# Kernel optimization log

Hardware: AMD Instinct MI355X
Metric: run time of the kernel (lower is better)

## Reference

```python
import jax, jax.numpy as jnp
import numpy as np

B, C, H, W = 2, 512, 64, 64


def conv1x1(x, w, b):
    # x: [B,C,H,W], w: [O,C], b: [O]
    return jnp.einsum('bchw,oc->bohw', x, w) + b[None, :, None, None]


def setup_inputs() -> dict:
    key = jax.random.key(0)
    ks = jax.random.split(key, 20)
    d = {
        'visSegF': jax.random.normal(ks[0], (B, C, H, W), jnp.float32),
        'irSegF': jax.random.normal(ks[1], (B, C, H, W), jnp.float32),
        'x_vis_p': jax.random.normal(ks[2], (B, C, H, W), jnp.float32),
        'x_ir_p': jax.random.normal(ks[3], (B, C, H, W), jnp.float32),
    }
    names = ['q_rd', 'k_rd', 'v_rd', 'q_dr', 'k_dr', 'v_dr']
    for i, n in enumerate(names):
        d['W' + n] = jax.random.normal(ks[4 + 2 * i], (C, C), jnp.float32) * 0.02
        d['b' + n] = jax.random.normal(ks[5 + 2 * i], (C,), jnp.float32) * 0.01
    # gamma params are init-zero in torch; use small nonzero values so both paths contribute
    d['gamma_rd'] = jax.random.normal(ks[16], (1,), jnp.float32) * 0.1
    d['gamma_dr'] = jax.random.normal(ks[17], (1,), jnp.float32) * 0.1
    return d


def reference(visSegF, irSegF, x_vis_p, x_ir_p,
              Wq_rd, bq_rd, Wk_rd, bk_rd, Wv_rd, bv_rd,
              Wq_dr, bq_dr, Wk_dr, bk_dr, Wv_dr, bv_dr,
              gamma_rd, gamma_dr):
    b, c, h, w = x_vis_p.shape
    n = h * w

    # rd path: query from x_vis_p, key from visSegF, value from x_ir_p (sr_ratio == 1 branch)
    q_vis = conv1x1(x_vis_p, Wq_rd, bq_rd).reshape(b, c, n)      # [B,C,N]
    key_d = conv1x1(visSegF, Wk_rd, bk_rd).reshape(b, c, -1)     # [B,C,M]
    val_d = conv1x1(x_ir_p, Wv_rd, bv_rd).reshape(b, c, -1)      # [B,C,M]
    # torch: softmax(bmm(q^T, k), dim=1) -> softmax over query positions (axis=1)
    attn_rd = jax.nn.softmax(jnp.einsum('bcn,bcm->bnm', q_vis, key_d), axis=1)
    out_rd = jnp.einsum('bcm,bnm->bcn', val_d, attn_rd).reshape(b, c, h, w)

    # dr path: query from x_ir_p, key/value from irSegF
    q_ir = conv1x1(x_ir_p, Wq_dr, bq_dr).reshape(b, c, n)
    key_r = conv1x1(irSegF, Wk_dr, bk_dr).reshape(b, c, -1)
    val_r = conv1x1(irSegF, Wv_dr, bv_dr).reshape(b, c, -1)
    attn_dr = jax.nn.softmax(jnp.einsum('bcn,bcm->bnm', q_ir, key_r), axis=1)
    out_dr = jnp.einsum('bcm,bnm->bcn', val_r, attn_dr).reshape(b, c, h, w)

    out_rd = jax.nn.relu(gamma_rd[0] * out_rd + x_vis_p)
    out_dr = jax.nn.relu(gamma_dr[0] * out_dr + x_ir_p)
    return (out_rd, out_dr)
```

## Files before the change

### kernel.cpp

```cpp
#include <hip/hip_runtime.h>
#include <stdint.h>


typedef __attribute__((ext_vector_type(8))) __bf16 bf16x8;
typedef __attribute__((ext_vector_type(4))) float f32x4;

__device__ __forceinline__ unsigned short f2bf(float f) {
  union { float f; unsigned u; } v; v.f = f;
  unsigned r = v.u + 0x7FFFu + ((v.u >> 16) & 1u);
  return (unsigned short)(r >> 16);
}
__device__ __forceinline__ float bf2f(unsigned short b) {
  union { unsigned u; float f; } v; v.u = ((unsigned)b) << 16;
  return v.f;
}

__device__ __forceinline__ void async_copy16(const unsigned short* g,
                                             unsigned short* l) {
  __builtin_amdgcn_global_load_lds(
      (const __attribute__((address_space(1))) unsigned int*)g,
      (__attribute__((address_space(3))) unsigned int*)l, 16, 0, 0);
}

template <int NSUB>
__device__ __forceinline__ void gemm_core(
    const unsigned short* __restrict__ Ag, const unsigned short* __restrict__ Bg,
    int K, int lda, int ldb, int rowbase, int colbase,
    f32x4 (&acc)[4][4], unsigned short* Al, unsigned short* Bl) {
  const int tid = threadIdx.x;
  const int w = tid >> 6, lane = tid & 63;
  const int quad = lane >> 4, l16 = lane & 15;
  const int wm = (w >> 1) << 6, wn = (w & 1) << 6;
  const int rbase = (w << 5) + (lane >> 2);

  for (int k0 = 0; k0 < K; k0 += 32 * NSUB) {
#pragma unroll
    for (int half = 0; half < NSUB; ++half) {
      int kh = k0 + (half << 5);
      unsigned short* Ah = Al + (half << 12);
      unsigned short* Bh = Bl + (half << 12);
#pragma unroll
      for (int i = 0; i < 2; ++i) {
        int rloc = rbase + (i << 4);
        int cg = (lane & 3) ^ ((rloc >> 1) & 3);
        int koff = kh + (cg << 3);
        int ldsoff = ((w << 5) + (i << 4)) << 5;
        async_copy16(Ag + (size_t)(rowbase + rloc) * lda + koff, Ah + ldsoff);
        async_copy16(Bg + (size_t)(colbase + rloc) * ldb + koff, Bh + ldsoff);
      }
    }
    __syncthreads();
#pragma unroll
    for (int half = 0; half < NSUB; ++half) {
      unsigned short* Ah = Al + (half << 12);
      unsigned short* Bh = Bl + (half << 12);
      bf16x8 af[4], bfr[4];
#pragma unroll
      for (int i = 0; i < 4; ++i) {
        int r = wm + (i << 4) + l16;
        af[i] = *(const bf16x8*)(Ah + (r << 5) + ((quad ^ ((r >> 1) & 3)) << 3));
      }
#pragma unroll
      for (int j = 0; j < 4; ++j) {
        int r = wn + (j << 4) + l16;
        bfr[j] = *(const bf16x8*)(Bh + (r << 5) + ((quad ^ ((r >> 1) & 3)) << 3));
      }
#pragma unroll
      for (int i = 0; i < 4; ++i)
#pragma unroll
        for (int j = 0; j < 4; ++j)
          acc[i][j] = __builtin_amdgcn_mfma_f32_16x16x32_bf16(af[i], bfr[j], acc[i][j], 0, 0, 0);
    }
    __syncthreads();
  }
}

struct WArgs { const float* src[6]; unsigned short* dst[6]; };
__global__ __launch_bounds__(256) void k_cvtw(WArgs a) {
  int z = blockIdx.y;
  int i = (blockIdx.x * 256 + threadIdx.x) << 3;
  const float* s = a.src[z] + i;
  float4 v0 = *(const float4*)s;
  float4 v1 = *(const float4*)(s + 4);
  unsigned short pk[8] = {f2bf(v0.x), f2bf(v0.y), f2bf(v0.z), f2bf(v0.w),
                          f2bf(v1.x), f2bf(v1.y), f2bf(v1.z), f2bf(v1.w)};
  *(int4*)(a.dst[z] + i) = *(int4*)pk;
}

struct TArgs { const float* src[4]; unsigned short* dst[4]; };
__global__ __launch_bounds__(256) void k_tcvt(TArgs a) {
  __shared__ float tile[32][68];
  int z = blockIdx.z;
  const float* src = a.src[z >> 1] + (size_t)(z & 1) * (512 * 4096);
  unsigned short* dst = a.dst[z >> 1] + (size_t)(z & 1) * (4096 * 512);
  int n0 = blockIdx.x << 6;
  int c0 = blockIdx.y << 5;
  int tid = threadIdx.x;
  int q = tid & 15, r0 = tid >> 4;
#pragma unroll
  for (int pass = 0; pass < 2; ++pass) {
    int r = r0 + (pass << 4);
    *(float4*)&tile[r][q << 2] =
        *(const float4*)(src + (size_t)(c0 + r) * 4096 + n0 + (q << 2));
  }
  __syncthreads();
  int j = tid >> 2, c8 = (tid & 3) << 3;
  unsigned short pk[8];
#pragma unroll
  for (int k = 0; k < 8; ++k) pk[k] = f2bf(tile[c8 + k][j]);
  *(int4*)(dst + (size_t)(n0 + j) * 512 + c0 + c8) = *(int4*)pk;
}

struct ConvArgs {
  const unsigned short* W[12];
  const unsigned short* X[12];
  const float* bias[12];
  unsigned short* out[12];
  int trans[12];
};
__global__ __launch_bounds__(256) void k_conv(ConvArgs a) {
  __shared__ unsigned short sh[16384];
  int z = blockIdx.z;
  int trans = a.trans[z];
  int rowbase = (trans ? blockIdx.x : blockIdx.y) << 7;
  int colbase = (trans ? blockIdx.y : blockIdx.x) << 7;
  const unsigned short* Ag = trans ? a.X[z] : a.W[z];
  const unsigned short* Bg = trans ? a.W[z] : a.X[z];
  f32x4 acc[4][4];
#pragma unroll
  for (int i = 0; i < 4; ++i)
#pragma unroll
    for (int j = 0; j < 4; ++j) acc[i][j] = (f32x4){0.f, 0.f, 0.f, 0.f};
  gemm_core<2>(Ag, Bg, 512, 512, 512, rowbase, colbase, acc, sh, sh + 8192);

  const int tid = threadIdx.x, w = tid >> 6, lane = tid & 63;
  const int quad = lane >> 4, l16 = lane & 15;
  const int wm = (w >> 1) << 6, wn = (w & 1) << 6;
  const float* bias = a.bias[z];
  unsigned short* out = a.out[z];
  if (trans) {
    float bo[4];
#pragma unroll
    for (int j = 0; j < 4; ++j) bo[j] = bias[colbase + wn + (j << 4) + l16];
#pragma unroll
    for (int i = 0; i < 4; ++i) {
      int n0 = rowbase + wm + (i << 4) + (quad << 2);
#pragma unroll
      for (int j = 0; j < 4; ++j) {
        int o = colbase + wn + (j << 4) + l16;
        out[(size_t)(n0 + 0) * 512 + o] = f2bf(acc[i][j].x + bo[j]);
        out[(size_t)(n0 + 1) * 512 + o] = f2bf(acc[i][j].y + bo[j]);
        out[(size_t)(n0 + 2) * 512 + o] = f2bf(acc[i][j].z + bo[j]);
        out[(size_t)(n0 + 3) * 512 + o] = f2bf(acc[i][j].w + bo[j]);
      }
    }
  } else {
#pragma unroll
    for (int i = 0; i < 4; ++i) {
      int o0 = rowbase + wm + (i << 4) + (quad << 2);
      float b0 = bias[o0], b1 = bias[o0 + 1], b2 = bias[o0 + 2], b3 = bias[o0 + 3];
#pragma unroll
      for (int j = 0; j < 4; ++j) {
        int n = colbase + wn + (j << 4) + l16;
        out[(size_t)(o0 + 0) * 4096 + n] = f2bf(acc[i][j].x + b0);
        out[(size_t)(o0 + 1) * 4096 + n] = f2bf(acc[i][j].y + b1);
        out[(size_t)(o0 + 2) * 4096 + n] = f2bf(acc[i][j].z + b2);
        out[(size_t)(o0 + 3) * 4096 + n] = f2bf(acc[i][j].w + b3);
      }
    }
  }
}

struct QKArgs {
  const unsigned short* Q[4]; const unsigned short* K[4]; unsigned short* T[4];
  float* pz;
};
__global__ __launch_bounds__(256) void k_qk(QKArgs a) {
  __shared__ unsigned short sh[16384];
  int z = blockIdx.z;
  int nbase = blockIdx.y << 7;
  int mbase = blockIdx.x << 7;
  f32x4 acc[4][4];
#pragma unroll
  for (int i = 0; i < 4; ++i)
#pragma unroll
    for (int j = 0; j < 4; ++j) acc[i][j] = (f32x4){0.f, 0.f, 0.f, 0.f};
  gemm_core<2>(a.Q[z], a.K[z], 512, 512, 512, nbase, mbase, acc, sh, sh + 8192);

  const int tid = threadIdx.x, w = tid >> 6, lane = tid & 63;
  const int quad = lane >> 4, l16 = lane & 15;
  const int wm = (w >> 1) << 6, wn = (w & 1) << 6;
  unsigned short* T = a.T[z];
  float sjv[4] = {0.f, 0.f, 0.f, 0.f};
#pragma unroll
  for (int i = 0; i < 4; ++i) {
    int n0 = nbase + wm + (i << 4) + (quad << 2);
#pragma unroll
    for (int j = 0; j < 4; ++j) {
      int m = mbase + wn + (j << 4) + l16;
      float e0 = __expf(acc[i][j].x);
      float e1 = __expf(acc[i][j].y);
      float e2 = __expf(acc[i][j].z);
      float e3 = __expf(acc[i][j].w);
      T[(size_t)(n0 + 0) * 4096 + m] = f2bf(e0);
      T[(size_t)(n0 + 1) * 4096 + m] = f2bf(e1);
      T[(size_t)(n0 + 2) * 4096 + m] = f2bf(e2);
      T[(size_t)(n0 + 3) * 4096 + m] = f2bf(e3);
      sjv[j] += e0 + e1 + e2 + e3;
    }
  }
  float* red = (float*)sh;
#pragma unroll
  for (int j = 0; j < 4; ++j) {
    float s = sjv[j];
    s += __shfl_xor(s, 16, 64);
    s += __shfl_xor(s, 32, 64);
    if (quad == 0) red[(w << 6) + (j << 4) + l16] = s;
  }
  __syncthreads();
  if (tid < 128) {
    int h = tid >> 6, t = tid & 63;
    float S = red[(h << 6) + t] + red[((h + 2) << 6) + t];
    int m = mbase + (h << 6) + t;
    a.pz[((z << 5) + blockIdx.y) * 4096 + m] = S;
  }
}

__global__ __launch_bounds__(256) void k_stats2(const float* __restrict__ pz,
                                                float* __restrict__ c) {
  int m = (blockIdx.x << 8) + threadIdx.x;
  int z = blockIdx.y;
  float S = 0.f;
#pragma unroll
  for (int k = 0; k < 32; ++k) S += pz[((z << 5) + k) * 4096 + m];
  c[z * 4096 + m] = 1.f / S;
}

struct VSArgs { unsigned short* V[4]; const float* c; };
__global__ __launch_bounds__(256) void k_vscale(VSArgs a) {
  int z = blockIdx.y;
  int t = blockIdx.x * 256 + threadIdx.x;
  int m0 = (t & 511) << 3;
  int row = t >> 9;
  unsigned short* p = a.V[z] + (size_t)row * 4096 + m0;
  const float* cz = a.c + z * 4096 + m0;
  int4 raw = *(const int4*)p;
  unsigned short* u = (unsigned short*)&raw;
#pragma unroll
  for (int j = 0; j < 8; ++j) u[j] = f2bf(bf2f(u[j]) * cz[j]);
  *(int4*)p = raw;
}

struct PVArgs {
  const unsigned short* V[4];
  const unsigned short* P[4];
  const float* resid[4];
  const float* gamma[4];
  float* out[4];
};
__global__ __launch_bounds__(256) void k_pv(PVArgs a) {
  __shared__ unsigned short sh[32768];
  int z = blockIdx.z;
  int rowbase = blockIdx.y << 7;
  int colbase = blockIdx.x << 7;
  f32x4 acc[4][4];
#pragma unroll
  for (int i = 0; i < 4; ++i)
#pragma unroll
    for (int j = 0; j < 4; ++j) acc[i][j] = (f32x4){0.f, 0.f, 0.f, 0.f};
  gemm_core<4>(a.V[z], a.P[z], 4096, 4096, 4096, rowbase, colbase, acc, sh, sh + 16384);

  const int tid = threadIdx.x, w = tid >> 6, lane = tid & 63;
  const int quad = lane >> 4, l16 = lane & 15;
  const int wm = (w >> 1) << 6, wn = (w & 1) << 6;
  float g = a.gamma[z][0];
  const float* R = a.resid[z];
  float* O = a.out[z];
#pragma unroll
  for (int i = 0; i < 4; ++i) {
    int c0 = rowbase + wm + (i << 4) + (quad << 2);
#pragma unroll
    for (int j = 0; j < 4; ++j) {
      int n = colbase + wn + (j << 4) + l16;
      O[(size_t)(c0 + 0) * 4096 + n] = fmaxf(g * acc[i][j].x + R[(size_t)(c0 + 0) * 4096 + n], 0.f);
      O[(size_t)(c0 + 1) * 4096 + n] = fmaxf(g * acc[i][j].y + R[(size_t)(c0 + 1) * 4096 + n], 0.f);
      O[(size_t)(c0 + 2) * 4096 + n] = fmaxf(g * acc[i][j].z + R[(size_t)(c0 + 2) * 4096 + n], 0.f);
      O[(size_t)(c0 + 3) * 4096 + n] = fmaxf(g * acc[i][j].w + R[(size_t)(c0 + 3) * 4096 + n], 0.f);
    }
  }
}

extern "C" void kernel_launch(void* const* d_in, const int* in_sizes, int n_in,
                              void* d_out, int out_size, void* d_ws, size_t ws_size,
                              hipStream_t stream) {
  char* ws = (char*)d_ws;
  unsigned short* wb  = (unsigned short*)(ws);
  unsigned short* xt  = (unsigned short*)(ws + 3145728);
  unsigned short* qkv = (unsigned short*)(ws + 36700160);
  unsigned short* tt  = (unsigned short*)(ws + 87031808);
  float* pz  = (float*)(ws + 3145728);
  float* cb  = (float*)(ws + 3145728 + 2097152);

  WArgs wa;
  for (int i = 0; i < 6; ++i) {
    wa.src[i] = (const float*)d_in[4 + 2 * i];
    wa.dst[i] = wb + (size_t)i * 262144;
  }
  k_cvtw<<<dim3(128, 6), 256, 0, stream>>>(wa);

  TArgs ta;
  for (int ai = 0; ai < 4; ++ai) {
    ta.src[ai] = (const float*)d_in[ai];
    ta.dst[ai] = xt + (size_t)ai * 4194304;
  }
  k_tcvt<<<dim3(64, 16, 8), 256, 0, stream>>>(ta);

  const int srcArr[6] = {2, 0, 3, 3, 1, 1};
  const int trans[6] = {1, 1, 0, 1, 1, 0};
  ConvArgs ca;
  for (int ci = 0; ci < 6; ++ci)
    for (int b = 0; b < 2; ++b) {
      int zz = ci * 2 + b;
      ca.W[zz] = wb + (size_t)ci * 262144;
      ca.X[zz] = xt + (size_t)srcArr[ci] * 4194304 + (size_t)b * 2097152;
      ca.bias[zz] = (const float*)d_in[5 + 2 * ci];
      ca.out[zz] = qkv + (size_t)zz * 2097152;
      ca.trans[zz] = trans[ci];
    }
  k_conv<<<dim3(32, 4, 12), 256, 0, stream>>>(ca);

  QKArgs qa;
  for (int path = 0; path < 2; ++path)
    for (int b = 0; b < 2; ++b) {
      int zz = path * 2 + b;
      qa.Q[zz] = qkv + (size_t)((path * 3 + 0) * 2 + b) * 2097152;
      qa.K[zz] = qkv + (size_t)((path * 3 + 1) * 2 + b) * 2097152;
      qa.T[zz] = tt + (size_t)zz * 16777216;
    }
  qa.pz = pz;
  k_qk<<<dim3(32, 32, 4), 256, 0, stream>>>(qa);

  k_stats2<<<dim3(16, 4), 256, 0, stream>>>(pz, cb);

  VSArgs va;
  for (int path = 0; path < 2; ++path)
    for (int b = 0; b < 2; ++b)
      va.V[path * 2 + b] = qkv + (size_t)((path * 3 + 2) * 2 + b) * 2097152;
  va.c = cb;
  k_vscale<<<dim3(1024, 4), 256, 0, stream>>>(va);

  PVArgs pa;
  const float* resid_src[2] = {(const float*)d_in[2], (const float*)d_in[3]};
  const float* gsrc[2] = {(const float*)d_in[16], (const float*)d_in[17]};
  for (int path = 0; path < 2; ++path)
    for (int b = 0; b < 2; ++b) {
      int zz = path * 2 + b;
      pa.V[zz] = qkv + (size_t)((path * 3 + 2) * 2 + b) * 2097152;
      pa.P[zz] = tt + (size_t)zz * 16777216;
      pa.resid[zz] = resid_src[path] + (size_t)b * 2097152;
      pa.gamma[zz] = gsrc[path];
      pa.out[zz] = (float*)d_out + (size_t)zz * 2097152;
    }
  k_pv<<<dim3(32, 4, 4), 256, 0, stream>>>(pa);
}
```

Baseline: 380.2 us.

## Deepen GEMM pipeline to four stages and fuse softmax stats into V scaling

The conv and QK GEMM kernels now use a four-stage shared-memory pipeline instead of two, doubling LDS per block so more k-tiles of loads are in flight. The column-sum reduction kernel and the V rescaling kernel are merged into one kernel that computes reciprocal sums into shared memory and then scales the matching V columns. This removes one launch and the round trip of the reciprocal array through global memory. The trade-offs are lower occupancy from the larger LDS footprint, and a merged kernel with only 64 blocks, each looping over 512 rows.

```diff
diff --git a/kernel.cpp b/kernel.cpp
--- a/kernel.cpp
+++ b/kernel.cpp
@@ -119,7 +119,7 @@
   int trans[12];
 };
 __global__ __launch_bounds__(256) void k_conv(ConvArgs a) {
-  __shared__ unsigned short sh[16384];
+  __shared__ unsigned short sh[32768];
   int z = blockIdx.z;
   int trans = a.trans[z];
   int rowbase = (trans ? blockIdx.x : blockIdx.y) << 7;
@@ -131,7 +131,7 @@
   for (int i = 0; i < 4; ++i)
 #pragma unroll
     for (int j = 0; j < 4; ++j) acc[i][j] = (f32x4){0.f, 0.f, 0.f, 0.f};
-  gemm_core<2>(Ag, Bg, 512, 512, 512, rowbase, colbase, acc, sh, sh + 8192);
+  gemm_core<4>(Ag, Bg, 512, 512, 512, rowbase, colbase, acc, sh, sh + 16384);
 
   const int tid = threadIdx.x, w = tid >> 6, lane = tid & 63;
   const int quad = lane >> 4, l16 = lane & 15;
@@ -176,7 +176,7 @@
   float* pz;
 };
 __global__ __launch_bounds__(256) void k_qk(QKArgs a) {
-  __shared__ unsigned short sh[16384];
+  __shared__ unsigned short sh[32768];
   int z = blockIdx.z;
   int nbase = blockIdx.y << 7;
   int mbase = blockIdx.x << 7;
@@ -185,7 +185,7 @@
   for (int i = 0; i < 4; ++i)
 #pragma unroll
     for (int j = 0; j < 4; ++j) acc[i][j] = (f32x4){0.f, 0.f, 0.f, 0.f};
-  gemm_core<2>(a.Q[z], a.K[z], 512, 512, 512, nbase, mbase, acc, sh, sh + 8192);
+  gemm_core<4>(a.Q[z], a.K[z], 512, 512, 512, nbase, mbase, acc, sh, sh + 16384);
 
   const int tid = threadIdx.x, w = tid >> 6, lane = tid & 63;
   const int quad = lane >> 4, l16 = lane & 15;
@@ -226,29 +226,29 @@
   }
 }
 
-__global__ __launch_bounds__(256) void k_stats2(const float* __restrict__ pz,
-                                                float* __restrict__ c) {
-  int m = (blockIdx.x << 8) + threadIdx.x;
+struct VSArgs { unsigned short* V[4]; const float* pz; };
+__global__ __launch_bounds__(256) void k_vstats(VSArgs a) {
+  __shared__ float cl[256];
   int z = blockIdx.y;
+  int mbase = blockIdx.x << 8;
+  int m = mbase + threadIdx.x;
   float S = 0.f;
 #pragma unroll
-  for (int k = 0; k < 32; ++k) S += pz[((z << 5) + k) * 4096 + m];
-  c[z * 4096 + m] = 1.f / S;
-}
-
-struct VSArgs { unsigned short* V[4]; const float* c; };
-__global__ __launch_bounds__(256) void k_vscale(VSArgs a) {
-  int z = blockIdx.y;
-  int t = blockIdx.x * 256 + threadIdx.x;
-  int m0 = (t & 511) << 3;
-  int row = t >> 9;
-  unsigned short* p = a.V[z] + (size_t)row * 4096 + m0;
-  const float* cz = a.c + z * 4096 + m0;
-  int4 raw = *(const int4*)p;
-  unsigned short* u = (unsigned short*)&raw;
-#pragma unroll
-  for (int j = 0; j < 8; ++j) u[j] = f2bf(bf2f(u[j]) * cz[j]);
-  *(int4*)p = raw;
+  for (int k = 0; k < 32; ++k) S += a.pz[((z << 5) + k) * 4096 + m];
+  cl[threadIdx.x] = 1.f / S;
+  __syncthreads();
+  unsigned short* V = a.V[z];
+  int tm = (threadIdx.x & 31) << 3;
+  int r0 = threadIdx.x >> 5;
+  const float* cz = cl + tm;
+  for (int r = r0; r < 512; r += 8) {
+    unsigned short* p = V + (size_t)r * 4096 + mbase + tm;
+    int4 raw = *(const int4*)p;
+    unsigned short* u = (unsigned short*)&raw;
+#pragma unroll
+    for (int j = 0; j < 8; ++j) u[j] = f2bf(bf2f(u[j]) * cz[j]);
+    *(int4*)p = raw;
+  }
 }
 
 struct PVArgs {
@@ -299,7 +299,6 @@
   unsigned short* qkv = (unsigned short*)(ws + 36700160);
   unsigned short* tt  = (unsigned short*)(ws + 87031808);
   float* pz  = (float*)(ws + 3145728);
-  float* cb  = (float*)(ws + 3145728 + 2097152);
 
   WArgs wa;
   for (int i = 0; i < 6; ++i) {
@@ -340,14 +339,12 @@
   qa.pz = pz;
   k_qk<<<dim3(32, 32, 4), 256, 0, stream>>>(qa);
 
-  k_stats2<<<dim3(16, 4), 256, 0, stream>>>(pz, cb);
-
   VSArgs va;
   for (int path = 0; path < 2; ++path)
     for (int b = 0; b < 2; ++b)
       va.V[path * 2 + b] = qkv + (size_t)((path * 3 + 2) * 2 + b) * 2097152;
-  va.c = cb;
-  k_vscale<<<dim3(1024, 4), 256, 0, stream>>>(va);
+  va.pz = pz;
+  k_vstats<<<dim3(16, 4), 256, 0, stream>>>(va);
 
   PVArgs pa;
   const float* resid_src[2] = {(const float*)d_in[2], (const float*)d_in[3]};
```

New measurement: 426.5 us. 12.2% more time.
